# Optimization experiments

Hardware: AMD Instinct MI355X
Metric: run time of the kernel (lower is better)

## Reference

```python
import jax, jax.numpy as jnp
import numpy as np

R = 4  # num_relations
G = 256  # num graphs in batch


def rgcn_conv(x, W, root, b, src, dst, etype, num_nodes):
    # PyG RGCNConv (default aggr='mean'):
    # out_i = root @ x_i + b + sum_r mean_{j in N_r(i)} W_r @ x_j
    xr = jnp.einsum('ni,rio->rno', x, W)            # [R, N, O]
    m = xr[etype, src]                               # [E, O] per-edge messages
    seg = dst * R + etype                            # (node, relation) segment id
    ones = jnp.ones(etype.shape, dtype=x.dtype)
    cnt = jax.ops.segment_sum(ones, seg, num_segments=num_nodes * R)
    norm = 1.0 / jnp.maximum(cnt[seg], 1.0)          # 1/|N_r(i)| per edge
    agg = jax.ops.segment_sum(m * norm[:, None], dst, num_segments=num_nodes)
    return agg + x @ root + b


def forward(x, W1, root1, b1, W2, root2, b2, W3, root3, b3,
            Wf1, bf1, Wh, bh, Wl, bl, src, dst, etype, batch):
    N = x.shape[0]
    h = jax.nn.relu(rgcn_conv(x, W1, root1, b1, src, dst, etype, N))
    h = jax.nn.relu(rgcn_conv(h, W2, root2, b2, src, dst, etype, N))
    h = rgcn_conv(h, W3, root3, b3, src, dst, etype, N)        # [N, 64]
    g = jax.ops.segment_max(h, batch, num_segments=G)          # scatter_max pool [G, 64]
    # MLP head: 64 -> 128 -> 256 -> num_classes, ReLU, softmax(dim=1)
    g = jax.nn.relu(g @ Wf1 + bf1)
    g = jax.nn.relu(g @ Wh + bh)
    g = g @ Wl + bl
    return jax.nn.softmax(g, axis=1)


def setup_inputs() -> dict:
    key = jax.random.key(0)
    ks = jax.random.split(key, 20)
    N, E, num_classes = 100000, 1600000, 51

    def glorot(k, shape):
        fan_in, fan_out = shape[-2], shape[-1]
        s = jnp.sqrt(6.0 / (fan_in + fan_out))
        return jax.random.uniform(k, shape, jnp.float32, -s, s)

    x = jax.random.normal(ks[0], (N, 16), jnp.float32)
    edge_index = jax.random.randint(ks[1], (2, E), 0, N)
    edge_type = jax.random.randint(ks[2], (E,), 0, R)
    batch = (jnp.arange(N) * G) // N  # sorted, covers all G graphs

    inp = {
        'x': x, 'edge_index': edge_index, 'edge_type': edge_type, 'batch': batch,
        'W1': glorot(ks[3], (R, 16, 16)), 'root1': glorot(ks[4], (16, 16)), 'b1': jnp.zeros((16,)),
        'W2': glorot(ks[5], (R, 16, 32)), 'root2': glorot(ks[6], (16, 32)), 'b2': jnp.zeros((32,)),
        'W3': glorot(ks[7], (R, 32, 64)), 'root3': glorot(ks[8], (32, 64)), 'b3': jnp.zeros((64,)),
        'Wf1': glorot(ks[9], (64, 128)), 'bf1': jnp.zeros((128,)),
        'Wh': glorot(ks[10], (128, 256)), 'bh': jnp.zeros((256,)),
        'Wl': glorot(ks[11], (256, num_classes)), 'bl': jnp.zeros((num_classes,)),
    }
    return inp


def reference(x, W1, root1, b1, W2, root2, b2, W3, root3, b3,
              Wf1, bf1, Wh, bh, Wl, bl, edge_index, edge_type, batch):
    src, dst = edge_index[0], edge_index[1]
    return forward(x, W1, root1, b1, W2, root2, b2, W3, root3, b3,
                   Wf1, bf1, Wh, bh, Wl, bl, src, dst, etype=edge_type, batch=batch)
```

## Files before the change

### kernel.cpp

```cpp
#include <hip/hip_runtime.h>

#define RELS 4
#define NGRAPH 256
#define SCAN_BLK 2048

static inline size_t alignup(size_t x) { return (x + 255) & ~(size_t)255; }

__global__ void hist_kernel(const int* __restrict__ dst, const int* __restrict__ et,
                            int* __restrict__ hcnt, int E)
{
    int e = blockIdx.x * blockDim.x + threadIdx.x;
    if (e < E) atomicAdd(&hcnt[dst[e] * RELS + et[e]], 1);
}

__global__ __launch_bounds__(256)
void scan1_kernel(const int* __restrict__ in, int* __restrict__ excl,
                  int* __restrict__ bsum, int n)
{
    __shared__ int lds[256];
    int tid = threadIdx.x;
    int base = blockIdx.x * SCAN_BLK + tid * 8;
    int v[8];
    #pragma unroll
    for (int i = 0; i < 8; ++i) v[i] = (base + i < n) ? in[base + i] : 0;
    int run = 0;
    #pragma unroll
    for (int i = 0; i < 8; ++i) { int t = v[i]; v[i] = run; run += t; }
    lds[tid] = run;
    __syncthreads();
    for (int off = 1; off < 256; off <<= 1) {
        int t = (tid >= off) ? lds[tid - off] : 0;
        __syncthreads();
        lds[tid] += t;
        __syncthreads();
    }
    int ex = (tid > 0) ? lds[tid - 1] : 0;
    if (tid == 255) bsum[blockIdx.x] = lds[255];
    #pragma unroll
    for (int i = 0; i < 8; ++i) if (base + i < n) excl[base + i] = v[i] + ex;
}

__global__ __launch_bounds__(256)
void scan2_kernel(const int* __restrict__ bsum, int* __restrict__ boff, int nb)
{
    __shared__ int lds[256];
    int tid = threadIdx.x;
    lds[tid] = (tid < nb) ? bsum[tid] : 0;
    __syncthreads();
    for (int off = 1; off < 256; off <<= 1) {
        int t = (tid >= off) ? lds[tid - off] : 0;
        __syncthreads();
        lds[tid] += t;
        __syncthreads();
    }
    if (tid < nb) boff[tid] = (tid > 0) ? lds[tid - 1] : 0;
}

__global__ void scan3_kernel(const int* __restrict__ excl, const int* __restrict__ boff,
                             int* __restrict__ ptr, int* __restrict__ cursor,
                             int n, int total)
{
    int i = blockIdx.x * blockDim.x + threadIdx.x;
    if (i < n) {
        int v = excl[i] + boff[i / SCAN_BLK];
        ptr[i] = v;
        cursor[i] = v;
    }
    if (i == 0) ptr[n] = total;
}

__global__ void fill_pass_kernel(const int* __restrict__ src, const int* __restrict__ dst,
                                 const int* __restrict__ et,
                                 int* __restrict__ cursor, int* __restrict__ ssrc,
                                 int E, int lo, int hi)
{
    int e = blockIdx.x * blockDim.x + threadIdx.x;
    if (e < E) {
        int d = dst[e];
        if (d >= lo && d < hi) {
            int seg = d * RELS + et[e];
            int pos = atomicAdd(&cursor[seg], 1);
            ssrc[pos] = src[e];
        }
    }
}

template<int IN, int OUT, bool RELU, int LPN, int MINW>
__global__ __launch_bounds__(512, MINW)
void rgcn_layer_kernel(const float* __restrict__ feat,
                       const int* __restrict__ ptr, const int* __restrict__ ssrc,
                       const float* __restrict__ W, const float* __restrict__ root,
                       const float* __restrict__ bias,
                       float* __restrict__ hout, int n)
{
    constexpr int TPB = 512;
    constexpr int NPB = TPB / LPN;
    constexpr int K   = 4 * IN;
    constexpr int AGS = K + 1;
    constexpr int F4  = IN / 4;
    constexpr int Q   = OUT / LPN;
    constexpr int NB  = NPB / 64;

    static_assert(F4 == LPN, "one float4 slice per lane");

    __shared__ float agg[NPB * AGS];

    const int tid  = (int)threadIdx.x;
    const int nl   = tid / LPN;
    const int c4   = tid % LPN;
    const int node = (int)blockIdx.x * NPB + nl;

    const float4* fv = (const float4*)feat;

    if (node < n) {
        int4 p4  = *(const int4*)(ptr + (size_t)node * RELS);
        int b4v  = ptr[(size_t)node * RELS + RELS];
        const int b0 = p4.x, b1 = p4.y, b2 = p4.z, b3 = p4.w;

        float4 ac0 = {0.f, 0.f, 0.f, 0.f};
        float4 ac1 = ac0, ac2 = ac0, ac3 = ac0;

        auto accadd = [&](int ei, float4 v) {
            bool ge0 = ei >= b0, ge1 = ei >= b1, ge2 = ei >= b2,
                 ge3 = ei >= b3, lt4 = ei < b4v;
            float w0 = (ge0 && !ge1) ? 1.f : 0.f;
            float w1 = (ge1 && !ge2) ? 1.f : 0.f;
            float w2 = (ge2 && !ge3) ? 1.f : 0.f;
            float w3 = (ge3 && lt4) ? 1.f : 0.f;
            ac0.x = fmaf(v.x, w0, ac0.x); ac0.y = fmaf(v.y, w0, ac0.y);
            ac0.z = fmaf(v.z, w0, ac0.z); ac0.w = fmaf(v.w, w0, ac0.w);
            ac1.x = fmaf(v.x, w1, ac1.x); ac1.y = fmaf(v.y, w1, ac1.y);
            ac1.z = fmaf(v.z, w1, ac1.z); ac1.w = fmaf(v.w, w1, ac1.w);
            ac2.x = fmaf(v.x, w2, ac2.x); ac2.y = fmaf(v.y, w2, ac2.y);
            ac2.z = fmaf(v.z, w2, ac2.z); ac2.w = fmaf(v.w, w2, ac2.w);
            ac3.x = fmaf(v.x, w3, ac3.x); ac3.y = fmaf(v.y, w3, ac3.y);
            ac3.z = fmaf(v.z, w3, ac3.z); ac3.w = fmaf(v.w, w3, ac3.w);
        };

        const int4* sv4 = (const int4*)ssrc;
        const int e0 = b0 & ~7;
        for (int e = e0; e < b4v; e += 8) {
            int4 ia = sv4[(e >> 2) + 0];
            int4 ib = sv4[(e >> 2) + 1];
            int s[8] = {ia.x, ia.y, ia.z, ia.w, ib.x, ib.y, ib.z, ib.w};
            float4 v[8];
            #pragma unroll
            for (int j = 0; j < 8; ++j) {
                int ss = s[j];
                ss = (ss < 0) ? 0 : ((ss >= n) ? 0 : ss);
                v[j] = fv[(size_t)ss * F4 + c4];
            }
            #pragma unroll
            for (int j = 0; j < 8; ++j) accadd(e + j, v[j]);
        }

        float nm0 = 1.0f / fmaxf((float)(b1 - b0), 1.0f);
        float nm1 = 1.0f / fmaxf((float)(b2 - b1), 1.0f);
        float nm2 = 1.0f / fmaxf((float)(b3 - b2), 1.0f);
        float nm3 = 1.0f / fmaxf((float)(b4v - b3), 1.0f);

        float* arow = &agg[nl * AGS];
        int kb = c4 * 4;
        arow[0 * IN + kb + 0] = ac0.x * nm0; arow[0 * IN + kb + 1] = ac0.y * nm0;
        arow[0 * IN + kb + 2] = ac0.z * nm0; arow[0 * IN + kb + 3] = ac0.w * nm0;
        arow[1 * IN + kb + 0] = ac1.x * nm1; arow[1 * IN + kb + 1] = ac1.y * nm1;
        arow[1 * IN + kb + 2] = ac1.z * nm1; arow[1 * IN + kb + 3] = ac1.w * nm1;
        arow[2 * IN + kb + 0] = ac2.x * nm2; arow[2 * IN + kb + 1] = ac2.y * nm2;
        arow[2 * IN + kb + 2] = ac2.z * nm2; arow[2 * IN + kb + 3] = ac2.w * nm2;
        arow[3 * IN + kb + 0] = ac3.x * nm3; arow[3 * IN + kb + 1] = ac3.y * nm3;
        arow[3 * IN + kb + 2] = ac3.z * nm3; arow[3 * IN + kb + 3] = ac3.w * nm3;
    }
    __syncthreads();

    const int wv   = __builtin_amdgcn_readfirstlane(tid >> 6);
    const int lane = tid & 63;
    const int nb   = wv % NB;
    const int cg   = wv / NB;
    const int ln   = nb * 64 + lane;
    const int cn   = (int)blockIdx.x * NPB + ln;
    const int cnc  = (cn < n) ? cn : (n - 1);

    const float* __restrict__ wq = W    + cg * Q;
    const float* __restrict__ rq = root + cg * Q;
    const float* __restrict__ bq = bias + cg * Q;
    const float* arow = &agg[ln * AGS];

    float acc[Q];
    #pragma unroll
    for (int o = 0; o < Q; ++o) acc[o] = bq[o];

    #pragma unroll 4
    for (int k = 0; k < K; ++k) {
        float m = arow[k];
        const float* wr = wq + (size_t)k * OUT;
        #pragma unroll
        for (int o = 0; o < Q; ++o) acc[o] += m * wr[o];
    }
    #pragma unroll
    for (int j = 0; j < F4; ++j) {
        float4 v = fv[(size_t)cnc * F4 + j];
        #pragma unroll
        for (int c = 0; c < 4; ++c) {
            float m = (&v.x)[c];
            const float* wr = rq + (size_t)(j * 4 + c) * OUT;
            #pragma unroll
            for (int o = 0; o < Q; ++o) acc[o] += m * wr[o];
        }
    }

    if (cn < n) {
        float* ho = hout + (size_t)cn * OUT + cg * Q;
        #pragma unroll
        for (int o = 0; o < Q; o += 4) {
            float4 v;
            v.x = RELU ? fmaxf(acc[o + 0], 0.f) : acc[o + 0];
            v.y = RELU ? fmaxf(acc[o + 1], 0.f) : acc[o + 1];
            v.z = RELU ? fmaxf(acc[o + 2], 0.f) : acc[o + 2];
            v.w = RELU ? fmaxf(acc[o + 3], 0.f) : acc[o + 3];
            *(float4*)(ho + o) = v;
        }
    }
}

__device__ inline int lower_bound_i(const int* a, int n, int key)
{
    int lo = 0, hi = n;
    while (lo < hi) { int mid = (lo + hi) >> 1; if (a[mid] < key) lo = mid + 1; else hi = mid; }
    return lo;
}

__global__ __launch_bounds__(256)
void pool_kernel(const float* __restrict__ h3, const int* __restrict__ batch,
                 float* __restrict__ gpool, int n)
{
    int g = blockIdx.x;
    int t = threadIdx.x;
    int ch = t & 63, q = t >> 6;

    int start = lower_bound_i(batch, n, g);
    int end   = lower_bound_i(batch, n, g + 1);

    float m = -INFINITY;
    for (int r = start + q; r < end; r += 4)
        m = fmaxf(m, h3[(size_t)r * 64 + ch]);

    __shared__ float red[4][64];
    red[q][ch] = m;
    __syncthreads();
    if (q == 0) {
        m = fmaxf(fmaxf(red[0][ch], red[1][ch]), fmaxf(red[2][ch], red[3][ch]));
        gpool[g * 64 + ch] = m;
    }
}

__global__ __launch_bounds__(256)
void mlp_kernel(const float* __restrict__ gpool,
                const float* __restrict__ Wf1, const float* __restrict__ bf1,
                const float* __restrict__ Wh,  const float* __restrict__ bh,
                const float* __restrict__ Wl,  const float* __restrict__ bl,
                float* __restrict__ out)
{
    __shared__ float gin[64];
    __shared__ float f1[128];
    __shared__ float f2[256];
    __shared__ float lg[51];
    int g = blockIdx.x, t = threadIdx.x;

    if (t < 64) gin[t] = gpool[g * 64 + t];
    __syncthreads();

    if (t < 128) {
        float a = bf1[t];
        #pragma unroll 8
        for (int k = 0; k < 64; ++k) a += gin[k] * Wf1[k * 128 + t];
        f1[t] = fmaxf(a, 0.f);
    }
    __syncthreads();

    {
        float a = bh[t];
        #pragma unroll 8
        for (int k = 0; k < 128; ++k) a += f1[k] * Wh[k * 256 + t];
        f2[t] = fmaxf(a, 0.f);
    }
    __syncthreads();

    if (t < 51) {
        float a = bl[t];
        #pragma unroll 8
        for (int k = 0; k < 256; ++k) a += f2[k] * Wl[k * 51 + t];
        lg[t] = a;
    }
    __syncthreads();

    if (t == 0) {
        float m = lg[0];
        for (int i = 1; i < 51; ++i) m = fmaxf(m, lg[i]);
        float ssum = 0.f;
        for (int i = 0; i < 51; ++i) { float e = __expf(lg[i] - m); lg[i] = e; ssum += e; }
        float inv = 1.0f / ssum;
        for (int i = 0; i < 51; ++i) out[g * 51 + i] = lg[i] * inv;
    }
}

extern "C" void kernel_launch(void* const* d_in, const int* in_sizes, int n_in,
                              void* d_out, int out_size, void* d_ws, size_t ws_size,
                              hipStream_t stream)
{
    const float* x    = (const float*)d_in[0];
    const int*   ei   = (const int*)d_in[1];
    const int*   et   = (const int*)d_in[2];
    const int*   batch= (const int*)d_in[3];
    const float* W1   = (const float*)d_in[4];
    const float* r1   = (const float*)d_in[5];
    const float* b1   = (const float*)d_in[6];
    const float* W2   = (const float*)d_in[7];
    const float* r2   = (const float*)d_in[8];
    const float* b2   = (const float*)d_in[9];
    const float* W3   = (const float*)d_in[10];
    const float* r3   = (const float*)d_in[11];
    const float* b3   = (const float*)d_in[12];
    const float* Wf1  = (const float*)d_in[13];
    const float* bf1  = (const float*)d_in[14];
    const float* Wh   = (const float*)d_in[15];
    const float* bh   = (const float*)d_in[16];
    const float* Wl   = (const float*)d_in[17];
    const float* bl   = (const float*)d_in[18];

    const int N = in_sizes[0] / 16;
    const int E = in_sizes[2];
    const int NSEG = N * RELS;
    const int NBLK = (NSEG + SCAN_BLK - 1) / SCAN_BLK;
    const int* srcp = ei;
    const int* dstp = ei + E;

    char* ws = (char*)d_ws;
    size_t off = 0;
    int*   hcnt   = (int*)(ws + off);   off += alignup((size_t)NSEG * 4);
    int*   ptr    = (int*)(ws + off);   off += alignup((size_t)(NSEG + 1) * 4);
    int*   excl   = (int*)(ws + off);   off += alignup((size_t)NSEG * 4);
    int*   bsum   = (int*)(ws + off);   off += alignup(256 * 4);
    int*   boff   = (int*)(ws + off);   off += alignup(256 * 4);
    int*   cursor = (int*)(ws + off);   off += alignup((size_t)NSEG * 4);
    int*   ssrc   = (int*)(ws + off);   off += alignup((size_t)E * 4 + 64);
    float* h1     = (float*)(ws + off); off += alignup((size_t)N * 16 * 4);
    float* h2     = (float*)(ws + off); off += alignup((size_t)N * 32 * 4);
    float* h3     = (float*)(ws + off); off += alignup((size_t)N * 64 * 4);
    float* gpool  = (float*)(ws + off); off += alignup((size_t)NGRAPH * 64 * 4);
    (void)ws_size; (void)n_in; (void)out_size;

    (void)hipMemsetAsync(hcnt, 0, (size_t)NSEG * 4, stream);
    hist_kernel<<<(E + 255) / 256, 256, 0, stream>>>(dstp, et, hcnt, E);
    scan1_kernel<<<NBLK, 256, 0, stream>>>(hcnt, excl, bsum, NSEG);
    scan2_kernel<<<1, 256, 0, stream>>>(bsum, boff, NBLK);
    scan3_kernel<<<(NSEG + 255) / 256, 256, 0, stream>>>(excl, boff, ptr, cursor, NSEG, E);

    {
        const int P = 4;
        for (int p = 0; p < P; ++p) {
            int lo = (int)((long long)N * p / P);
            int hi = (int)((long long)N * (p + 1) / P);
            fill_pass_kernel<<<(E + 255) / 256, 256, 0, stream>>>(
                srcp, dstp, et, cursor, ssrc, E, lo, hi);
        }
    }

    rgcn_layer_kernel<16, 16, true, 4, 6><<<(N + 127) / 128, 512, 0, stream>>>(
        x, ptr, ssrc, W1, r1, b1, h1, N);
    rgcn_layer_kernel<16, 32, true, 4, 6><<<(N + 127) / 128, 512, 0, stream>>>(
        h1, ptr, ssrc, W2, r2, b2, h2, N);
    rgcn_layer_kernel<32, 64, false, 8, 6><<<(N + 63) / 64, 512, 0, stream>>>(
        h2, ptr, ssrc, W3, r3, b3, h3, N);

    pool_kernel<<<NGRAPH, 256, 0, stream>>>(h3, batch, gpool, N);

    mlp_kernel<<<NGRAPH, 256, 0, stream>>>(gpool, Wf1, bf1, Wh, bh, Wl, bl, (float*)d_out);
}
```

Before: 364.0 us.

## Use 64 nodes per block and replace aligned int4 index loads with clamped scalar loads

Result: faster. 337.7 us (-7.2%).

```diff
diff --git a/kernel.cpp b/kernel.cpp
--- a/kernel.cpp
+++ b/kernel.cpp
@@ -85,23 +85,23 @@
     }
 }
 
-template<int IN, int OUT, bool RELU, int LPN, int MINW>
-__global__ __launch_bounds__(512, MINW)
+template<int IN, int OUT, bool RELU, int TPB, int MINW>
+__global__ __launch_bounds__(TPB, MINW)
 void rgcn_layer_kernel(const float* __restrict__ feat,
                        const int* __restrict__ ptr, const int* __restrict__ ssrc,
                        const float* __restrict__ W, const float* __restrict__ root,
                        const float* __restrict__ bias,
                        float* __restrict__ hout, int n)
 {
-    constexpr int TPB = 512;
+    constexpr int LPN = IN / 4;
     constexpr int NPB = TPB / LPN;
     constexpr int K   = 4 * IN;
     constexpr int AGS = K + 1;
     constexpr int F4  = IN / 4;
-    constexpr int Q   = OUT / LPN;
-    constexpr int NB  = NPB / 64;
-
-    static_assert(F4 == LPN, "one float4 slice per lane");
+    constexpr int WAVES = TPB / 64;
+    constexpr int Q   = OUT / WAVES;
+
+    static_assert(NPB == 64, "one node per lane in phase 2");
 
     __shared__ float agg[NPB * AGS];
 
@@ -121,9 +121,8 @@
         float4 ac1 = ac0, ac2 = ac0, ac3 = ac0;
 
         auto accadd = [&](int ei, float4 v) {
-            bool ge0 = ei >= b0, ge1 = ei >= b1, ge2 = ei >= b2,
-                 ge3 = ei >= b3, lt4 = ei < b4v;
-            float w0 = (ge0 && !ge1) ? 1.f : 0.f;
+            bool ge1 = ei >= b1, ge2 = ei >= b2, ge3 = ei >= b3, lt4 = ei < b4v;
+            float w0 = (!ge1 && lt4) ? 1.f : 0.f;
             float w1 = (ge1 && !ge2) ? 1.f : 0.f;
             float w2 = (ge2 && !ge3) ? 1.f : 0.f;
             float w3 = (ge3 && lt4) ? 1.f : 0.f;
@@ -137,19 +136,18 @@
             ac3.z = fmaf(v.z, w3, ac3.z); ac3.w = fmaf(v.w, w3, ac3.w);
         };
 
-        const int4* sv4 = (const int4*)ssrc;
-        const int e0 = b0 & ~7;
-        for (int e = e0; e < b4v; e += 8) {
-            int4 ia = sv4[(e >> 2) + 0];
-            int4 ib = sv4[(e >> 2) + 1];
-            int s[8] = {ia.x, ia.y, ia.z, ia.w, ib.x, ib.y, ib.z, ib.w};
+        const int last = b4v - 1;
+        for (int e = b0; e < b4v; e += 8) {
+            int idx[8];
+            #pragma unroll
+            for (int j = 0; j < 8; ++j) {
+                int ee = e + j;
+                idx[j] = ssrc[(ee < b4v) ? ee : last];
+            }
             float4 v[8];
             #pragma unroll
-            for (int j = 0; j < 8; ++j) {
-                int ss = s[j];
-                ss = (ss < 0) ? 0 : ((ss >= n) ? 0 : ss);
-                v[j] = fv[(size_t)ss * F4 + c4];
-            }
+            for (int j = 0; j < 8; ++j)
+                v[j] = fv[(size_t)idx[j] * F4 + c4];
             #pragma unroll
             for (int j = 0; j < 8; ++j) accadd(e + j, v[j]);
         }
@@ -172,18 +170,15 @@
     }
     __syncthreads();
 
-    const int wv   = __builtin_amdgcn_readfirstlane(tid >> 6);
+    const int cg   = __builtin_amdgcn_readfirstlane(tid >> 6);
     const int lane = tid & 63;
-    const int nb   = wv % NB;
-    const int cg   = wv / NB;
-    const int ln   = nb * 64 + lane;
-    const int cn   = (int)blockIdx.x * NPB + ln;
+    const int cn   = (int)blockIdx.x * NPB + lane;
     const int cnc  = (cn < n) ? cn : (n - 1);
 
     const float* __restrict__ wq = W    + cg * Q;
     const float* __restrict__ rq = root + cg * Q;
     const float* __restrict__ bq = bias + cg * Q;
-    const float* arow = &agg[ln * AGS];
+    const float* arow = &agg[lane * AGS];
 
     float acc[Q];
     #pragma unroll
@@ -342,7 +337,7 @@
     int*   bsum   = (int*)(ws + off);   off += alignup(256 * 4);
     int*   boff   = (int*)(ws + off);   off += alignup(256 * 4);
     int*   cursor = (int*)(ws + off);   off += alignup((size_t)NSEG * 4);
-    int*   ssrc   = (int*)(ws + off);   off += alignup((size_t)E * 4 + 64);
+    int*   ssrc   = (int*)(ws + off);   off += alignup((size_t)E * 4);
     float* h1     = (float*)(ws + off); off += alignup((size_t)N * 16 * 4);
     float* h2     = (float*)(ws + off); off += alignup((size_t)N * 32 * 4);
     float* h3     = (float*)(ws + off); off += alignup((size_t)N * 64 * 4);
@@ -365,11 +360,11 @@
         }
     }
 
-    rgcn_layer_kernel<16, 16, true, 4, 6><<<(N + 127) / 128, 512, 0, stream>>>(
+    rgcn_layer_kernel<16, 16, true, 256, 6><<<(N + 63) / 64, 256, 0, stream>>>(
         x, ptr, ssrc, W1, r1, b1, h1, N);
-    rgcn_layer_kernel<16, 32, true, 4, 6><<<(N + 127) / 128, 512, 0, stream>>>(
+    rgcn_layer_kernel<16, 32, true, 256, 6><<<(N + 63) / 64, 256, 0, stream>>>(
         h1, ptr, ssrc, W2, r2, b2, h2, N);
-    rgcn_layer_kernel<32, 64, false, 8, 6><<<(N + 63) / 64, 512, 0, stream>>>(
+    rgcn_layer_kernel<32, 64, false, 512, 6><<<(N + 63) / 64, 512, 0, stream>>>(
         h2, ptr, ssrc, W3, r3, b3, h3, N);
 
     pool_kernel<<<NGRAPH, 256, 0, stream>>>(h3, batch, gpool, N);
```
